# Kernel optimization log

Hardware: AMD Instinct MI355X
Metric: run time of the kernel (lower is better)

## Reference

```python
import jax, jax.numpy as jnp
import numpy as np


def setup_inputs() -> dict:
    key = jax.random.key(0)
    ks = jax.random.split(key, 6)
    B, T, D, H = 32, 2048, 1024, 1024
    s = jax.random.normal(ks[0], (1, B, D), dtype=jnp.float32)
    h = jax.random.normal(ks[1], (B, T, D), dtype=jnp.float32)
    mask = jax.random.randint(ks[2], (B, T), 0, 2, dtype=jnp.int32)
    W = jax.random.normal(ks[3], (D, H), dtype=jnp.float32) * (6.0 / (D + H)) ** 0.5
    U = jax.random.normal(ks[4], (D, H), dtype=jnp.float32) * (6.0 / (D + H)) ** 0.5
    v = jax.random.normal(ks[5], (H, 1), dtype=jnp.float32) * (6.0 / (H + 1)) ** 0.5
    return {"s": s, "h": h, "mask": mask, "W": W, "U": U, "v": v}


def reference(s, h, mask, W, U, v):
    # mask-fill encoder states: zero out padded timesteps
    m = (mask != 0)[:, :, None]            # (B, T, 1)
    h = jnp.where(m, h, 0.0)               # (B, T, D)
    s_t = jnp.transpose(s, (1, 0, 2))      # (B, 1, D)
    proj_s = s_t @ W                       # (B, 1, H)
    proj_h = h @ U                         # (B, T, H)
    energy = jnp.tanh(proj_s + proj_h) @ v  # (B, T, 1)
    energy = jnp.where(m, energy, -1e9)
    score = jax.nn.softmax(energy, axis=1)  # softmax over time
    context = jnp.sum(score * h, axis=1)    # (B, D)
    return context
```

## Files before the change

kernel.cpp:

```cpp
#include <hip/hip_runtime.h>
#include <hip/hip_fp16.h>
#include <math.h>

#define BB 32
#define TT 2048
#define DD 1024
#define HH 1024
#define MM (BB*TT)

typedef _Float16 half8 __attribute__((ext_vector_type(8)));
typedef float f32x4 __attribute__((ext_vector_type(4)));

__device__ __forceinline__ float tanh_fast(float x) {
    float cx = fminf(fmaxf(x, -10.0f), 10.0f);
    float e2 = __expf(2.0f * cx);
    return (e2 - 1.0f) / (e2 + 1.0f);
}

__global__ void cast_h_kernel(const float* __restrict__ h,
                              _Float16* __restrict__ h16) {
    const long i0 = ((long)blockIdx.x * 256 + threadIdx.x) * 8;
    const float4 f0 = *(const float4*)(h + i0);
    const float4 f1 = *(const float4*)(h + i0 + 4);
    half8 o;
    o[0] = (_Float16)f0.x; o[1] = (_Float16)f0.y;
    o[2] = (_Float16)f0.z; o[3] = (_Float16)f0.w;
    o[4] = (_Float16)f1.x; o[5] = (_Float16)f1.y;
    o[6] = (_Float16)f1.z; o[7] = (_Float16)f1.w;
    *(half8*)(h16 + i0) = o;
}

__global__ void prep_ut_kernel(const float* __restrict__ U,
                               _Float16* __restrict__ Ut) {
    __shared__ float tile[32][33];
    const int bx = blockIdx.x, by = blockIdx.y;
    const int tx = threadIdx.x & 31, ty = threadIdx.x >> 5;
#pragma unroll
    for (int j = 0; j < 4; ++j) {
        const int k = by * 32 + ty + j * 8;
        tile[ty + j * 8][tx] = U[(long)k * HH + bx * 32 + tx];
    }
    __syncthreads();
#pragma unroll
    for (int j = 0; j < 4; ++j) {
        const int n = bx * 32 + ty + j * 8;
        Ut[(long)n * DD + by * 32 + tx] = (_Float16)tile[tx][ty + j * 8];
    }
}

__global__ void prep_ps_kernel(const float* __restrict__ s,
                               const float* __restrict__ W,
                               float* __restrict__ ps,
                               float* __restrict__ out) {
    const int nseg = blockIdx.x, b = blockIdx.y;
    const int n = nseg * 256 + threadIdx.x;
    __shared__ float ss[DD];
#pragma unroll
    for (int j = 0; j < 4; ++j)
        ss[threadIdx.x + j * 256] = s[b * DD + threadIdx.x + j * 256];
    out[b * HH + n] = 0.0f;
    __syncthreads();
    float a0 = 0.f, a1 = 0.f, a2 = 0.f, a3 = 0.f;
#pragma unroll 4
    for (int d = 0; d < DD; d += 4) {
        a0 += ss[d + 0] * W[(long)(d + 0) * HH + n];
        a1 += ss[d + 1] * W[(long)(d + 1) * HH + n];
        a2 += ss[d + 2] * W[(long)(d + 2) * HH + n];
        a3 += ss[d + 3] * W[(long)(d + 3) * HH + n];
    }
    ps[b * HH + n] = (a0 + a1) + (a2 + a3);
}

#define Bb_M 128
#define Bb_N 128
#define Bb_K 32
#define AP   40

template <bool A16>
__global__ __launch_bounds__(256)
void energy_gemm_kernel(const float* __restrict__ h32,
                        const _Float16* __restrict__ h16,
                        const _Float16* __restrict__ Ut,
                        const float* __restrict__ ps,
                        const float* __restrict__ v,
                        float* __restrict__ epart) {
    __shared__ _Float16 As[Bb_M][AP];
    __shared__ _Float16 Bs[Bb_N][AP];
    __shared__ float ps_s[Bb_N];
    __shared__ float v_s[Bb_N];

    const int nt = blockIdx.x;
    const int mt = blockIdx.y;
    const int m0 = mt * Bb_M;
    const int n0 = nt * Bb_N;
    const int b  = m0 >> 11;
    const int tid  = threadIdx.x;
    const int wave = tid >> 6;
    const int lane = tid & 63;
    const int wm = wave >> 1;
    const int wn = wave & 1;

    if (tid < Bb_N) {
        ps_s[tid] = ps[b * HH + n0 + tid];
        v_s[tid]  = v[n0 + tid];
    }

    const int arow = tid >> 1;
    const int aseg = (tid & 1) * 16;
    const float*    ap32 = h32 + (long)(m0 + arow) * DD + aseg;
    const _Float16* ap16 = h16 + (long)(m0 + arow) * DD + aseg;
    const _Float16* bp   = Ut  + (long)(n0 + arow) * DD + aseg;

    f32x4 acc[4][4];
#pragma unroll
    for (int i = 0; i < 4; ++i)
#pragma unroll
        for (int j = 0; j < 4; ++j) acc[i][j] = (f32x4)0.0f;

    const int lk = (lane >> 4) * 8;
    const int lr = lane & 15;

#pragma unroll 1
    for (int k0 = 0; k0 < DD; k0 += Bb_K) {
        half8 a0, a1;
        if (A16) {
            a0 = *(const half8*)(ap16 + k0);
            a1 = *(const half8*)(ap16 + k0 + 8);
        } else {
            const float4 f0 = *(const float4*)(ap32 + k0);
            const float4 f1 = *(const float4*)(ap32 + k0 + 4);
            const float4 f2 = *(const float4*)(ap32 + k0 + 8);
            const float4 f3 = *(const float4*)(ap32 + k0 + 12);
            a0[0] = (_Float16)f0.x; a0[1] = (_Float16)f0.y;
            a0[2] = (_Float16)f0.z; a0[3] = (_Float16)f0.w;
            a0[4] = (_Float16)f1.x; a0[5] = (_Float16)f1.y;
            a0[6] = (_Float16)f1.z; a0[7] = (_Float16)f1.w;
            a1[0] = (_Float16)f2.x; a1[1] = (_Float16)f2.y;
            a1[2] = (_Float16)f2.z; a1[3] = (_Float16)f2.w;
            a1[4] = (_Float16)f3.x; a1[5] = (_Float16)f3.y;
            a1[6] = (_Float16)f3.z; a1[7] = (_Float16)f3.w;
        }
        const half8 bv0 = *(const half8*)(bp + k0);
        const half8 bv1 = *(const half8*)(bp + k0 + 8);

        __syncthreads();

        *(half8*)&As[arow][aseg]     = a0;
        *(half8*)&As[arow][aseg + 8] = a1;
        *(half8*)&Bs[arow][aseg]     = bv0;
        *(half8*)&Bs[arow][aseg + 8] = bv1;

        __syncthreads();

        half8 af[4], bf[4];
#pragma unroll
        for (int tm = 0; tm < 4; ++tm)
            af[tm] = *(const half8*)&As[wm * 64 + tm * 16 + lr][lk];
#pragma unroll
        for (int tn = 0; tn < 4; ++tn)
            bf[tn] = *(const half8*)&Bs[wn * 64 + tn * 16 + lr][lk];
#pragma unroll
        for (int tm = 0; tm < 4; ++tm)
#pragma unroll
            for (int tn = 0; tn < 4; ++tn)
                acc[tm][tn] = __builtin_amdgcn_mfma_f32_16x16x32_f16(
                    af[tm], bf[tn], acc[tm][tn], 0, 0, 0);
    }

    float part[4][4];
#pragma unroll
    for (int tm = 0; tm < 4; ++tm) {
#pragma unroll
        for (int r = 0; r < 4; ++r) {
            float p = 0.f;
#pragma unroll
            for (int tn = 0; tn < 4; ++tn) {
                const int cl = wn * 64 + tn * 16 + lr;
                p += v_s[cl] * tanh_fast(acc[tm][tn][r] + ps_s[cl]);
            }
            part[tm][r] = p;
        }
    }
#pragma unroll
    for (int off = 1; off < 16; off <<= 1)
#pragma unroll
        for (int tm = 0; tm < 4; ++tm)
#pragma unroll
            for (int r = 0; r < 4; ++r)
                part[tm][r] += __shfl_xor(part[tm][r], off, 64);

    if ((lane & 15) == 0) {
        const int slot = nt * 2 + wn;
#pragma unroll
        for (int tm = 0; tm < 4; ++tm)
#pragma unroll
            for (int r = 0; r < 4; ++r) {
                const int row = m0 + wm * 64 + tm * 16 + (lane >> 4) * 4 + r;
                epart[(long)slot * MM + row] = part[tm][r];
            }
    }
}

__global__ void softmax_kernel(const float* __restrict__ epart,
                               const int* __restrict__ mask,
                               float* __restrict__ score) {
    const int b = blockIdx.x;
    const int tid = threadIdx.x;
    float e[8];
    float mx = -1e30f;
#pragma unroll
    for (int i = 0; i < 8; ++i) {
        const int t = i * 256 + tid;
        const long row = (long)b * TT + t;
        float sum = 0.f;
#pragma unroll
        for (int p = 0; p < 16; ++p) sum += epart[(long)p * MM + row];
        if (mask[row] == 0) sum = -1e9f;
        e[i] = sum;
        mx = fmaxf(mx, sum);
    }
#pragma unroll
    for (int off = 32; off > 0; off >>= 1) mx = fmaxf(mx, __shfl_xor(mx, off, 64));
    __shared__ float r4[4];
    if ((tid & 63) == 0) r4[tid >> 6] = mx;
    __syncthreads();
    mx = fmaxf(fmaxf(r4[0], r4[1]), fmaxf(r4[2], r4[3]));

    float tot = 0.f;
#pragma unroll
    for (int i = 0; i < 8; ++i) { e[i] = expf(e[i] - mx); tot += e[i]; }
#pragma unroll
    for (int off = 32; off > 0; off >>= 1) tot += __shfl_xor(tot, off, 64);
    __shared__ float s4[4];
    __syncthreads();
    if ((tid & 63) == 0) s4[tid >> 6] = tot;
    __syncthreads();
    tot = s4[0] + s4[1] + s4[2] + s4[3];
    const float inv = 1.0f / tot;
#pragma unroll
    for (int i = 0; i < 8; ++i)
        score[(long)b * TT + i * 256 + tid] = e[i] * inv;
}

template <bool A16>
__global__ void context_kernel(const float* __restrict__ h32,
                               const _Float16* __restrict__ h16,
                               const float* __restrict__ score,
                               float* __restrict__ out) {
    const int tc = blockIdx.x;
    const int b  = blockIdx.y;
    const int d0 = threadIdx.x * 8;
    float a[8];
#pragma unroll
    for (int j = 0; j < 8; ++j) a[j] = 0.f;
    for (int i = 0; i < 128; ++i) {
        const int t = tc * 128 + i;
        const float sc = score[(long)b * TT + t];
        if (sc != 0.0f) {
            if (A16) {
                const half8 hv = *(const half8*)(h16 + ((long)(b * TT + t)) * DD + d0);
#pragma unroll
                for (int j = 0; j < 8; ++j) a[j] += sc * (float)hv[j];
            } else {
                const float4 h0 = *(const float4*)(h32 + ((long)(b * TT + t)) * DD + d0);
                const float4 h1 = *(const float4*)(h32 + ((long)(b * TT + t)) * DD + d0 + 4);
                a[0] += sc * h0.x; a[1] += sc * h0.y; a[2] += sc * h0.z; a[3] += sc * h0.w;
                a[4] += sc * h1.x; a[5] += sc * h1.y; a[6] += sc * h1.z; a[7] += sc * h1.w;
            }
        }
    }
#pragma unroll
    for (int j = 0; j < 8; ++j) atomicAdd(&out[b * DD + d0 + j], a[j]);
}

extern "C" void kernel_launch(void* const* d_in, const int* in_sizes, int n_in,
                              void* d_out, int out_size, void* d_ws, size_t ws_size,
                              hipStream_t stream) {
    const float* s    = (const float*)d_in[0];
    const float* h    = (const float*)d_in[1];
    const int*   mask = (const int*)  d_in[2];
    const float* W    = (const float*)d_in[3];
    const float* U    = (const float*)d_in[4];
    const float* v    = (const float*)d_in[5];
    float* out = (float*)d_out;

    const size_t sz_h16 = (size_t)BB * TT * DD * sizeof(_Float16);
    const size_t sz_ut  = (size_t)HH * DD * sizeof(_Float16);
    const size_t sz_ps  = (size_t)BB * HH * sizeof(float);
    const size_t sz_ep  = (size_t)16 * MM * sizeof(float);
    const size_t sz_sc  = (size_t)BB * TT * sizeof(float);
    const bool use16 = ws_size >= sz_h16 + sz_ut + sz_ps + sz_ep + sz_sc;

    char* ws = (char*)d_ws;
    _Float16* h16 = (_Float16*)ws;
    size_t off = use16 ? sz_h16 : 0;
    _Float16* Ut  = (_Float16*)(ws + off); off += sz_ut;
    float*    ps  = (float*)(ws + off);    off += sz_ps;
    float*    ep  = (float*)(ws + off);    off += sz_ep;
    float*    scr = (float*)(ws + off);

    if (use16)
        cast_h_kernel<<<32768, 256, 0, stream>>>(h, h16);
    prep_ut_kernel<<<dim3(32, 32), 256, 0, stream>>>(U, Ut);
    prep_ps_kernel<<<dim3(4, 32), 256, 0, stream>>>(s, W, ps, out);
    if (use16) {
        energy_gemm_kernel<true><<<dim3(8, 512), 256, 0, stream>>>(h, h16, Ut, ps, v, ep);
        softmax_kernel<<<32, 256, 0, stream>>>(ep, mask, scr);
        context_kernel<true><<<dim3(16, 32), 128, 0, stream>>>(h, h16, scr, out);
    } else {
        energy_gemm_kernel<false><<<dim3(8, 512), 256, 0, stream>>>(h, h16, Ut, ps, v, ep);
        softmax_kernel<<<32, 256, 0, stream>>>(ep, mask, scr);
        context_kernel<false><<<dim3(16, 32), 128, 0, stream>>>(h, h16, scr, out);
    }
}
```

Before: 683.1 us.

## Compact unmasked rows and run energy GEMM only on valid timesteps

Builds a per-batch list of unmasked timesteps plus a tile table, then runs the energy GEMM only over tiles of those compacted rows. Softmax and scatter work in compacted index space, and the fp16 cast of h skips masked rows. Global-to-LDS direct loads replace the register-staged shared-memory fills in the GEMM. With about half the mask zero, this aims to remove roughly half the GEMM and cast traffic, at the cost of extra small kernels, gather-style row loads, an unpadded LDS layout that may cause bank conflicts, and dropping the fp32 fallback path for small workspaces.

```diff
diff --git a/kernel.cpp b/kernel.cpp
--- a/kernel.cpp
+++ b/kernel.cpp
@@ -17,17 +17,75 @@
     return (e2 - 1.0f) / (e2 + 1.0f);
 }
 
+__device__ __forceinline__ void load_lds16(const _Float16* g, _Float16* l) {
+    __builtin_amdgcn_global_load_lds(
+        (const __attribute__((address_space(1))) void*)g,
+        (__attribute__((address_space(3))) void*)l, 16, 0, 0);
+}
+
+__global__ void compact_kernel(const int* __restrict__ mask,
+                               int* __restrict__ rowlist,
+                               int* __restrict__ cnts) {
+    const int b = blockIdx.x, tid = threadIdx.x;
+    const int lane = tid & 63, w = tid >> 6;
+    const int* mb = mask + b * TT;
+    const int t0 = tid * 8;
+    int m[8], c = 0;
+#pragma unroll
+    for (int j = 0; j < 8; ++j) { m[j] = (mb[t0 + j] != 0); c += m[j]; }
+    int pref = c;
+#pragma unroll
+    for (int off = 1; off < 64; off <<= 1) {
+        int nv = __shfl_up(pref, off, 64);
+        if (lane >= off) pref += nv;
+    }
+    __shared__ int wsum[4];
+    if (lane == 63) wsum[w] = pref;
+    __syncthreads();
+    int wbase = 0;
+    for (int i = 0; i < w; ++i) wbase += wsum[i];
+    int pos = wbase + pref - c;
+#pragma unroll
+    for (int j = 0; j < 8; ++j)
+        if (m[j]) rowlist[b * TT + pos++] = t0 + j;
+    const int total = wsum[0] + wsum[1] + wsum[2] + wsum[3];
+    if (tid == 0) cnts[b] = total;
+    __syncthreads();
+    const int padded = ((total + 127) >> 7) << 7;
+    const int lastt = (total > 0) ? rowlist[b * TT + total - 1] : 0;
+    for (int ci = total + tid; ci < padded; ci += 256)
+        rowlist[b * TT + ci] = lastt;
+}
+
+__global__ void tiles_kernel(const int* __restrict__ cnts,
+                             int* __restrict__ tile_b,
+                             int* __restrict__ tile_ci,
+                             int* __restrict__ ntiles) {
+    if (threadIdx.x == 0) {
+        int tot = 0;
+        for (int b = 0; b < BB; ++b) {
+            const int nt = (cnts[b] + 127) >> 7;
+            for (int i = 0; i < nt; ++i) { tile_b[tot] = b; tile_ci[tot] = i * 128; ++tot; }
+        }
+        *ntiles = tot;
+    }
+}
+
 __global__ void cast_h_kernel(const float* __restrict__ h,
+                              const int* __restrict__ mask,
                               _Float16* __restrict__ h16) {
-    const long i0 = ((long)blockIdx.x * 256 + threadIdx.x) * 8;
-    const float4 f0 = *(const float4*)(h + i0);
-    const float4 f1 = *(const float4*)(h + i0 + 4);
+    const int row = blockIdx.x * 2 + (threadIdx.x >> 7);
+    if (mask[row] == 0) return;
+    const int c = (threadIdx.x & 127) * 8;
+    const long base = (long)row * DD + c;
+    const float4 f0 = *(const float4*)(h + base);
+    const float4 f1 = *(const float4*)(h + base + 4);
     half8 o;
     o[0] = (_Float16)f0.x; o[1] = (_Float16)f0.y;
     o[2] = (_Float16)f0.z; o[3] = (_Float16)f0.w;
     o[4] = (_Float16)f1.x; o[5] = (_Float16)f1.y;
     o[6] = (_Float16)f1.z; o[7] = (_Float16)f1.w;
-    *(half8*)(h16 + i0) = o;
+    *(half8*)(h16 + base) = o;
 }
 
 __global__ void prep_ut_kernel(const float* __restrict__ U,
@@ -36,80 +94,83 @@
     const int bx = blockIdx.x, by = blockIdx.y;
     const int tx = threadIdx.x & 31, ty = threadIdx.x >> 5;
 #pragma unroll
-    for (int j = 0; j < 4; ++j) {
-        const int k = by * 32 + ty + j * 8;
-        tile[ty + j * 8][tx] = U[(long)k * HH + bx * 32 + tx];
-    }
-    __syncthreads();
-#pragma unroll
-    for (int j = 0; j < 4; ++j) {
-        const int n = bx * 32 + ty + j * 8;
-        Ut[(long)n * DD + by * 32 + tx] = (_Float16)tile[tx][ty + j * 8];
-    }
+    for (int j = 0; j < 4; ++j)
+        tile[ty + j * 8][tx] = U[(long)(by * 32 + ty + j * 8) * HH + bx * 32 + tx];
+    __syncthreads();
+#pragma unroll
+    for (int j = 0; j < 4; ++j)
+        Ut[(long)(bx * 32 + ty + j * 8) * DD + by * 32 + tx] =
+            (_Float16)tile[tx][ty + j * 8];
 }
 
 __global__ void prep_ps_kernel(const float* __restrict__ s,
                                const float* __restrict__ W,
                                float* __restrict__ ps,
                                float* __restrict__ out) {
-    const int nseg = blockIdx.x, b = blockIdx.y;
+    const int b = blockIdx.x, nseg = blockIdx.y;
     const int n = nseg * 256 + threadIdx.x;
     __shared__ float ss[DD];
 #pragma unroll
     for (int j = 0; j < 4; ++j)
         ss[threadIdx.x + j * 256] = s[b * DD + threadIdx.x + j * 256];
-    out[b * HH + n] = 0.0f;
-    __syncthreads();
-    float a0 = 0.f, a1 = 0.f, a2 = 0.f, a3 = 0.f;
-#pragma unroll 4
-    for (int d = 0; d < DD; d += 4) {
-        a0 += ss[d + 0] * W[(long)(d + 0) * HH + n];
-        a1 += ss[d + 1] * W[(long)(d + 1) * HH + n];
-        a2 += ss[d + 2] * W[(long)(d + 2) * HH + n];
-        a3 += ss[d + 3] * W[(long)(d + 3) * HH + n];
-    }
-    ps[b * HH + n] = (a0 + a1) + (a2 + a3);
-}
-
-#define Bb_M 128
-#define Bb_N 128
+    out[b * DD + n] = 0.0f;
+    __syncthreads();
+    float a[8];
+#pragma unroll
+    for (int j = 0; j < 8; ++j) a[j] = 0.f;
+    for (int d = 0; d < DD; d += 8) {
+#pragma unroll
+        for (int j = 0; j < 8; ++j)
+            a[j] += ss[d + j] * W[(long)(d + j) * HH + n];
+    }
+    ps[b * HH + n] = ((a[0]+a[1])+(a[2]+a[3])) + ((a[4]+a[5])+(a[6]+a[7]));
+}
+
 #define Bb_K 32
-#define AP   40
-
-template <bool A16>
+
 __global__ __launch_bounds__(256)
-void energy_gemm_kernel(const float* __restrict__ h32,
-                        const _Float16* __restrict__ h16,
+void energy_gemm_kernel(const _Float16* __restrict__ h16,
                         const _Float16* __restrict__ Ut,
                         const float* __restrict__ ps,
                         const float* __restrict__ v,
+                        const int* __restrict__ rowlist,
+                        const int* __restrict__ tile_b,
+                        const int* __restrict__ tile_ci,
+                        const int* __restrict__ ntiles,
                         float* __restrict__ epart) {
-    __shared__ _Float16 As[Bb_M][AP];
-    __shared__ _Float16 Bs[Bb_N][AP];
-    __shared__ float ps_s[Bb_N];
-    __shared__ float v_s[Bb_N];
+    const int mt = blockIdx.y;
+    if (mt >= *ntiles) return;
+    __shared__ _Float16 As[128][32];
+    __shared__ _Float16 Bs[128][32];
+    __shared__ float ps_s[128];
+    __shared__ float v_s[128];
+    __shared__ int   rl[128];
 
     const int nt = blockIdx.x;
-    const int mt = blockIdx.y;
-    const int m0 = mt * Bb_M;
-    const int n0 = nt * Bb_N;
-    const int b  = m0 >> 11;
-    const int tid  = threadIdx.x;
-    const int wave = tid >> 6;
-    const int lane = tid & 63;
-    const int wm = wave >> 1;
-    const int wn = wave & 1;
-
-    if (tid < Bb_N) {
+    const int b   = tile_b[mt];
+    const int ci0 = tile_ci[mt];
+    const int n0  = nt * 128;
+    const int tid = threadIdx.x;
+    const int wave = tid >> 6, lane = tid & 63;
+    const int wm = wave >> 1, wn = wave & 1;
+
+    if (tid < 128) {
         ps_s[tid] = ps[b * HH + n0 + tid];
         v_s[tid]  = v[n0 + tid];
-    }
-
-    const int arow = tid >> 1;
-    const int aseg = (tid & 1) * 16;
-    const float*    ap32 = h32 + (long)(m0 + arow) * DD + aseg;
-    const _Float16* ap16 = h16 + (long)(m0 + arow) * DD + aseg;
-    const _Float16* bp   = Ut  + (long)(n0 + arow) * DD + aseg;
+        rl[tid]   = rowlist[b * TT + ci0 + tid];
+    }
+    __syncthreads();
+
+    const int srow = wave * 32 + (lane >> 2);
+    const int sseg = (lane & 3) * 8;
+    const _Float16* gA0 = h16 + ((long)b * TT + rl[srow])      * DD + sseg;
+    const _Float16* gA1 = h16 + ((long)b * TT + rl[srow + 16]) * DD + sseg;
+    const _Float16* gB0 = Ut + (long)(n0 + srow) * DD + sseg;
+    const _Float16* gB1 = gB0 + 16 * DD;
+    _Float16* lA0 = &As[wave * 32][0];
+    _Float16* lA1 = &As[wave * 32 + 16][0];
+    _Float16* lB0 = &Bs[wave * 32][0];
+    _Float16* lB1 = &Bs[wave * 32 + 16][0];
 
     f32x4 acc[4][4];
 #pragma unroll
@@ -122,34 +183,11 @@
 
 #pragma unroll 1
     for (int k0 = 0; k0 < DD; k0 += Bb_K) {
-        half8 a0, a1;
-        if (A16) {
-            a0 = *(const half8*)(ap16 + k0);
-            a1 = *(const half8*)(ap16 + k0 + 8);
-        } else {
-            const float4 f0 = *(const float4*)(ap32 + k0);
-            const float4 f1 = *(const float4*)(ap32 + k0 + 4);
-            const float4 f2 = *(const float4*)(ap32 + k0 + 8);
-            const float4 f3 = *(const float4*)(ap32 + k0 + 12);
-            a0[0] = (_Float16)f0.x; a0[1] = (_Float16)f0.y;
-            a0[2] = (_Float16)f0.z; a0[3] = (_Float16)f0.w;
-            a0[4] = (_Float16)f1.x; a0[5] = (_Float16)f1.y;
-            a0[6] = (_Float16)f1.z; a0[7] = (_Float16)f1.w;
-            a1[0] = (_Float16)f2.x; a1[1] = (_Float16)f2.y;
-            a1[2] = (_Float16)f2.z; a1[3] = (_Float16)f2.w;
-            a1[4] = (_Float16)f3.x; a1[5] = (_Float16)f3.y;
-            a1[6] = (_Float16)f3.z; a1[7] = (_Float16)f3.w;
-        }
-        const half8 bv0 = *(const half8*)(bp + k0);
-        const half8 bv1 = *(const half8*)(bp + k0 + 8);
-
         __syncthreads();
-
-        *(half8*)&As[arow][aseg]     = a0;
-        *(half8*)&As[arow][aseg + 8] = a1;
-        *(half8*)&Bs[arow][aseg]     = bv0;
-        *(half8*)&Bs[arow][aseg + 8] = bv1;
-
+        load_lds16(gA0 + k0, lA0);
+        load_lds16(gA1 + k0, lA1);
+        load_lds16(gB0 + k0, lB0);
+        load_lds16(gB1 + k0, lB1);
         __syncthreads();
 
         half8 af[4], bf[4];
@@ -195,27 +233,31 @@
         for (int tm = 0; tm < 4; ++tm)
 #pragma unroll
             for (int r = 0; r < 4; ++r) {
-                const int row = m0 + wm * 64 + tm * 16 + (lane >> 4) * 4 + r;
-                epart[(long)slot * MM + row] = part[tm][r];
+                const int ci = ci0 + wm * 64 + tm * 16 + (lane >> 4) * 4 + r;
+                epart[(long)slot * MM + b * TT + ci] = part[tm][r];
             }
     }
 }
 
 __global__ void softmax_kernel(const float* __restrict__ epart,
-                               const int* __restrict__ mask,
+                               const int* __restrict__ rowlist,
+                               const int* __restrict__ cnts,
                                float* __restrict__ score) {
-    const int b = blockIdx.x;
-    const int tid = threadIdx.x;
-    float e[8];
-    float mx = -1e30f;
+    const int b = blockIdx.x, tid = threadIdx.x;
+    const int cnt = cnts[b];
+    for (int t = tid; t < TT; t += 256) score[b * TT + t] = 0.0f;
+
+    float e[8], mx = -1e30f;
 #pragma unroll
     for (int i = 0; i < 8; ++i) {
-        const int t = i * 256 + tid;
-        const long row = (long)b * TT + t;
-        float sum = 0.f;
-#pragma unroll
-        for (int p = 0; p < 16; ++p) sum += epart[(long)p * MM + row];
-        if (mask[row] == 0) sum = -1e9f;
+        const int ci = i * 256 + tid;
+        float sum = -1e30f;
+        if (ci < cnt) {
+            sum = 0.f;
+#pragma unroll
+            for (int p = 0; p < 16; ++p)
+                sum += epart[(long)p * MM + b * TT + ci];
+        }
         e[i] = sum;
         mx = fmaxf(mx, sum);
     }
@@ -228,23 +270,27 @@
 
     float tot = 0.f;
 #pragma unroll
-    for (int i = 0; i < 8; ++i) { e[i] = expf(e[i] - mx); tot += e[i]; }
+    for (int i = 0; i < 8; ++i) {
+        const int ci = i * 256 + tid;
+        e[i] = (ci < cnt) ? __expf(e[i] - mx) : 0.0f;
+        tot += e[i];
+    }
 #pragma unroll
     for (int off = 32; off > 0; off >>= 1) tot += __shfl_xor(tot, off, 64);
     __shared__ float s4[4];
-    __syncthreads();
     if ((tid & 63) == 0) s4[tid >> 6] = tot;
     __syncthreads();
     tot = s4[0] + s4[1] + s4[2] + s4[3];
     const float inv = 1.0f / tot;
 #pragma unroll
-    for (int i = 0; i < 8; ++i)
-        score[(long)b * TT + i * 256 + tid] = e[i] * inv;
-}
-
-template <bool A16>
-__global__ void context_kernel(const float* __restrict__ h32,
-                               const _Float16* __restrict__ h16,
+    for (int i = 0; i < 8; ++i) {
+        const int ci = i * 256 + tid;
+        if (ci < cnt)
+            score[b * TT + rowlist[b * TT + ci]] = e[i] * inv;
+    }
+}
+
+__global__ void context_kernel(const _Float16* __restrict__ h16,
                                const float* __restrict__ score,
                                float* __restrict__ out) {
     const int tc = blockIdx.x;
@@ -257,16 +303,9 @@
         const int t = tc * 128 + i;
         const float sc = score[(long)b * TT + t];
         if (sc != 0.0f) {
-            if (A16) {
-                const half8 hv = *(const half8*)(h16 + ((long)(b * TT + t)) * DD + d0);
-#pragma unroll
-                for (int j = 0; j < 8; ++j) a[j] += sc * (float)hv[j];
-            } else {
-                const float4 h0 = *(const float4*)(h32 + ((long)(b * TT + t)) * DD + d0);
-                const float4 h1 = *(const float4*)(h32 + ((long)(b * TT + t)) * DD + d0 + 4);
-                a[0] += sc * h0.x; a[1] += sc * h0.y; a[2] += sc * h0.z; a[3] += sc * h0.w;
-                a[4] += sc * h1.x; a[5] += sc * h1.y; a[6] += sc * h1.z; a[7] += sc * h1.w;
-            }
+            const half8 hv = *(const half8*)(h16 + ((long)(b * TT + t)) * DD + d0);
+#pragma unroll
+            for (int j = 0; j < 8; ++j) a[j] += sc * (float)hv[j];
         }
     }
 #pragma unroll
@@ -284,32 +323,26 @@
     const float* v    = (const float*)d_in[5];
     float* out = (float*)d_out;
 
-    const size_t sz_h16 = (size_t)BB * TT * DD * sizeof(_Float16);
-    const size_t sz_ut  = (size_t)HH * DD * sizeof(_Float16);
-    const size_t sz_ps  = (size_t)BB * HH * sizeof(float);
-    const size_t sz_ep  = (size_t)16 * MM * sizeof(float);
-    const size_t sz_sc  = (size_t)BB * TT * sizeof(float);
-    const bool use16 = ws_size >= sz_h16 + sz_ut + sz_ps + sz_ep + sz_sc;
-
     char* ws = (char*)d_ws;
-    _Float16* h16 = (_Float16*)ws;
-    size_t off = use16 ? sz_h16 : 0;
-    _Float16* Ut  = (_Float16*)(ws + off); off += sz_ut;
-    float*    ps  = (float*)(ws + off);    off += sz_ps;
-    float*    ep  = (float*)(ws + off);    off += sz_ep;
-    float*    scr = (float*)(ws + off);
-
-    if (use16)
-        cast_h_kernel<<<32768, 256, 0, stream>>>(h, h16);
+    size_t off = 0;
+    _Float16* h16 = (_Float16*)(ws + off); off += (size_t)MM * DD * 2;
+    _Float16* Ut  = (_Float16*)(ws + off); off += (size_t)HH * DD * 2;
+    float*    ps  = (float*)(ws + off);    off += (size_t)BB * HH * 4;
+    float*    ep  = (float*)(ws + off);    off += (size_t)16 * MM * 4;
+    float*    scr = (float*)(ws + off);    off += (size_t)MM * 4;
+    int*      rlist = (int*)(ws + off);    off += (size_t)MM * 4;
+    int*      cnts  = (int*)(ws + off);    off += 64 * 4;
+    int*      tb    = (int*)(ws + off);    off += 512 * 4;
+    int*      tci   = (int*)(ws + off);    off += 512 * 4;
+    int*      ntl   = (int*)(ws + off);
+
+    compact_kernel<<<BB, 256, 0, stream>>>(mask, rlist, cnts);
+    tiles_kernel  <<<1, 64, 0, stream>>>(cnts, tb, tci, ntl);
+    cast_h_kernel <<<MM / 2, 256, 0, stream>>>(h, mask, h16);
     prep_ut_kernel<<<dim3(32, 32), 256, 0, stream>>>(U, Ut);
-    prep_ps_kernel<<<dim3(4, 32), 256, 0, stream>>>(s, W, ps, out);
-    if (use16) {
-        energy_gemm_kernel<true><<<dim3(8, 512), 256, 0, stream>>>(h, h16, Ut, ps, v, ep);
-        softmax_kernel<<<32, 256, 0, stream>>>(ep, mask, scr);
-        context_kernel<true><<<dim3(16, 32), 128, 0, stream>>>(h, h16, scr, out);
-    } else {
-        energy_gemm_kernel<false><<<dim3(8, 512), 256, 0, stream>>>(h, h16, Ut, ps, v, ep);
-        softmax_kernel<<<32, 256, 0, stream>>>(ep, mask, scr);
-        context_kernel<false><<<dim3(16, 32), 128, 0, stream>>>(h, h16, scr, out);
-    }
-}
+    prep_ps_kernel<<<dim3(32, 4), 256, 0, stream>>>(s, W, ps, out);
+    energy_gemm_kernel<<<dim3(8, 512), 256, 0, stream>>>(h16, Ut, ps, v,
+                                                         rlist, tb, tci, ntl, ep);
+    softmax_kernel<<<BB, 256, 0, stream>>>(ep, rlist, cnts, scr);
+    context_kernel<<<dim3(16, 32), 128, 0, stream>>>(h16, scr, out);
+}
```

Measured after the change: 561.2 us. -17.8%, faster.
